# Kernel tuning notes

Hardware: AMD Instinct MI355X
Metric: run time of the kernel (lower is better)

## Reference

```python
import jax, jax.numpy as jnp
import numpy as np

TAU = 1.0  # temperaturesa
GRID = 5   # torch.chunk(..., 5) along H and W


def _cam(X, gamma, tau):
    # Channel attention: energy = Xf Xf^T over spatial dim, with max-subtraction/negation trick.
    B, C, H, W = X.shape
    Xf = X.reshape(B, C, H * W)
    energy = jnp.einsum('bcn,bdn->bcd', Xf, Xf)                      # [B,C,C]
    energy_new = jnp.max(energy, axis=-1, keepdims=True) - energy
    attn = jax.nn.softmax(energy_new / tau, axis=-1)
    out = jnp.einsum('bcd,bdn->bcn', attn, Xf).reshape(B, C, H, W)
    return gamma * out + X


def _pam(X, Wq, bq, Wk, bk, Wv, bv, gamma, tau):
    # Position attention with 1x1-conv q/k/v (1x1 conv == channel matmul).
    B, C, H, W = X.shape
    N = H * W
    Xf = X.reshape(B, C, N)
    q = jnp.einsum('kc,bcn->bnk', Wq, Xf) + bq                        # [B,N,C//8]
    k = jnp.einsum('kc,bcn->bkn', Wk, Xf) + bk[None, :, None]         # [B,C//8,N]
    v = jnp.einsum('dc,bcn->bdn', Wv, Xf) + bv[None, :, None]         # [B,C,N]
    energy = jnp.einsum('bnk,bkm->bnm', q, k)                         # [B,N,N]
    attn = jax.nn.softmax(energy / tau, axis=-1)
    # torch: bmm(value, attention.permute(0,2,1)) -> out[b,d,m] = sum_n v[b,d,n]*attn[b,m,n]
    out = jnp.einsum('bdn,bmn->bdm', v, attn).reshape(B, C, H, W)
    return gamma * out + X


def _cka_loss(X, Y):
    # linear_CKA_loss: HKH centering done as K - rowmean - colmean + totalmean.
    def cgram(Z):
        K = Z @ Z.T                                                   # [B,B]
        rm = jnp.mean(K, axis=1, keepdims=True)
        cm = jnp.mean(K, axis=0, keepdims=True)
        return K - rm - cm + jnp.mean(K)
    cX, cY = cgram(X), cgram(Y)
    hsic = jnp.sum(cX * cY)
    v1 = jnp.sqrt(jnp.sum(cX * cX))
    v2 = jnp.sqrt(jnp.sum(cY * cY))
    return -jnp.log(jnp.abs(hsic / (v1 * v2)) + 1e-8)


def _grid_chunks(X, g=GRID):
    # 5x5 spatial tiling -> [g*g, B, C, H/g, W/g]
    B, C, H, W = X.shape
    h, w = H // g, W // g
    return X.reshape(B, C, g, h, g, w).transpose(2, 4, 0, 1, 3, 5).reshape(g * g, B, C, h, w)


def setup_inputs() -> dict:
    key = jax.random.key(0)
    ks = jax.random.split(key, 10)
    B, C, H, W = 16, 256, 80, 80
    Ck = C // 8
    return {
        'feat_S': jax.random.normal(ks[0], (B, C, H, W), jnp.float32),
        'feat_T': jax.random.normal(ks[1], (B, C, H, W), jnp.float32),
        'Wq': jax.random.normal(ks[2], (Ck, C), jnp.float32),
        'bq': jax.random.normal(ks[3], (Ck,), jnp.float32),
        'Wk': jax.random.normal(ks[4], (Ck, C), jnp.float32),
        'bk': jax.random.normal(ks[5], (Ck,), jnp.float32),
        'Wv': jax.random.normal(ks[6], (C, C), jnp.float32),
        'bv': jax.random.normal(ks[7], (C,), jnp.float32),
        'gammacam': jax.random.normal(ks[8], (1,), jnp.float32),
        'gammapam': jax.random.normal(ks[9], (1,), jnp.float32),
    }


def reference(feat_S, feat_T, Wq, bq, Wk, bk, Wv, bv, gammacam, gammapam):
    # feature_transform == 'separately_CAMgridPAM_CKA'
    tau = TAU
    pam = lambda X: _pam(X, Wq, bq, Wk, bk, Wv, bv, gammapam, tau)
    chunks_S = _grid_chunks(feat_S)                                   # [25,B,C,16,16]
    chunks_T = _grid_chunks(feat_T)
    pam_S = jax.vmap(pam)(chunks_S)
    pam_T = jax.vmap(pam)(chunks_T)
    nchunk, B = pam_S.shape[0], pam_S.shape[1]
    flat_S = pam_S.reshape(nchunk, B, -1)
    flat_T = pam_T.reshape(nchunk, B, -1)
    loss_PAM = jnp.mean(jax.vmap(_cka_loss)(flat_S, flat_T))          # sum/n == mean
    CAM_S = _cam(feat_S, gammacam, tau)
    CAM_T = _cam(feat_T, gammacam, tau)
    loss_CAM = _cka_loss(CAM_S.reshape(B, -1), CAM_T.reshape(B, -1))
    return (loss_CAM, loss_PAM)
```

## Files before the change

### kernel.cpp

```cpp
#include <hip/hip_runtime.h>


typedef short bf16x8 __attribute__((ext_vector_type(8)));
typedef float f32x4 __attribute__((ext_vector_type(4)));

constexpr int BB = 16;
constexpr int CH = 256;
constexpr int HW = 6400;
constexpr int IMW = 80;

__device__ __forceinline__ int lds_off(int row, int half, int k2) {
  return row * 128 + ((((half << 6)) | k2) ^ ((row & 7) << 4));
}

__device__ __forceinline__ bf16x8 frag_ld(const char* base, int row, int half, int lane) {
  int off = row * 128 + ((((half << 6)) | ((lane >> 4) << 4)) ^ ((lane & 7) << 4));
  return *(const bf16x8*)(base + off);
}

__device__ __forceinline__ void cvt2(float x, unsigned short& h, unsigned short& l) {
  unsigned u = __float_as_uint(x);
  h = (unsigned short)(u >> 16);
  float r = x - __uint_as_float(u & 0xffff0000u);
  l = (unsigned short)(__float_as_uint(r) >> 16);
}

__device__ __forceinline__ void cvt4(float4 v, ushort4& h, ushort4& l) {
  cvt2(v.x, h.x, l.x); cvt2(v.y, h.y, l.y);
  cvt2(v.z, h.z, l.z); cvt2(v.w, h.w, l.w);
}

__device__ __forceinline__ void cvt8(float4 v0, float4 v1, bf16x8& hi, bf16x8& lo) {
  unsigned short h, l;
  cvt2(v0.x, h, l); hi[0] = (short)h; lo[0] = (short)l;
  cvt2(v0.y, h, l); hi[1] = (short)h; lo[1] = (short)l;
  cvt2(v0.z, h, l); hi[2] = (short)h; lo[2] = (short)l;
  cvt2(v0.w, h, l); hi[3] = (short)h; lo[3] = (short)l;
  cvt2(v1.x, h, l); hi[4] = (short)h; lo[4] = (short)l;
  cvt2(v1.y, h, l); hi[5] = (short)h; lo[5] = (short)l;
  cvt2(v1.z, h, l); hi[6] = (short)h; lo[6] = (short)l;
  cvt2(v1.w, h, l); hi[7] = (short)h; lo[7] = (short)l;
}

__device__ __forceinline__ unsigned short bf_rnd(float x) {
  unsigned u = __float_as_uint(x);
  return (unsigned short)((u + 0x8000u) >> 16);
}

__global__ __launch_bounds__(1024) void cam_energy_k(const float* __restrict__ fS,
                                                     const float* __restrict__ fT,
                                                     float* __restrict__ part) {
  const int kc = blockIdx.x, b = blockIdx.y, t = blockIdx.z;
  const float* X = (t ? fT : fS) + (size_t)b * CH * HW;
  __shared__ unsigned short lds[2 * 256 * 64];
  const int tid = threadIdx.x, lane = tid & 63, w = tid >> 6;
  const int wr = w >> 2, wc = w & 3;
  const int r0 = tid >> 2, kq = tid & 3;
  const int half = kq >> 1, k2b = (kq & 1) * 32;
  const float* Xr = X + (size_t)r0 * HW + kc * 800 + kq * 16;
  f32x4 acc[4][4] = {};
  float4 v[4];
#pragma unroll
  for (int q = 0; q < 4; ++q) v[q] = *(const float4*)(Xr + q * 4);
  for (int it = 0; it < 13; ++it) {
    char* pb = (char*)lds + (it & 1) * 32768;
#pragma unroll
    for (int q = 0; q < 4; ++q) {
      ushort4 u;
      u.x = bf_rnd(v[q].x); u.y = bf_rnd(v[q].y);
      u.z = bf_rnd(v[q].z); u.w = bf_rnd(v[q].w);
      *(ushort4*)(pb + lds_off(r0, half, k2b + q * 8)) = u;
    }
    __syncthreads();
    float4 nv[4];
    if (it < 12) {
      const int nk = (it + 1) * 64;
      if (nk + kq * 16 < 800) {
        const float* Xn = Xr + nk;
#pragma unroll
        for (int q = 0; q < 4; ++q) nv[q] = *(const float4*)(Xn + q * 4);
      } else {
#pragma unroll
        for (int q = 0; q < 4; ++q) nv[q] = make_float4(0.f, 0.f, 0.f, 0.f);
      }
    }
#pragma unroll
    for (int h = 0; h < 2; ++h) {
      bf16x8 bh[4];
#pragma unroll
      for (int n = 0; n < 4; ++n)
        bh[n] = frag_ld(pb, wc * 64 + n * 16 + (lane & 15), h, lane);
#pragma unroll
      for (int m = 0; m < 4; ++m) {
        bf16x8 a = frag_ld(pb, wr * 64 + m * 16 + (lane & 15), h, lane);
#pragma unroll
        for (int n = 0; n < 4; ++n)
          acc[m][n] = __builtin_amdgcn_mfma_f32_16x16x32_bf16(a, bh[n], acc[m][n], 0, 0, 0);
      }
    }
#pragma unroll
    for (int q = 0; q < 4; ++q) v[q] = nv[q];
  }
  float* Eb = part + (((size_t)kc * 2 + t) * BB + b) * 65536;
#pragma unroll
  for (int m = 0; m < 4; ++m)
#pragma unroll
    for (int n = 0; n < 4; ++n) {
      int row = wr * 64 + m * 16 + ((lane >> 4) << 2);
      int col = wc * 64 + n * 16 + (lane & 15);
#pragma unroll
      for (int r2 = 0; r2 < 4; ++r2)
        Eb[(size_t)(row + r2) * 256 + col] = acc[m][n][r2];
    }
}

__global__ __launch_bounds__(64) void cam_softmax_k(float* __restrict__ part) {
  const int c = blockIdx.x, b = blockIdx.y, t = blockIdx.z;
  const size_t base = (((size_t)t * BB + b) * CH + c) * CH;
  const int lane = threadIdx.x;
  float4 x = make_float4(0.f, 0.f, 0.f, 0.f);
#pragma unroll
  for (int p = 0; p < 8; ++p) {
    float4 y = ((const float4*)(part + (size_t)p * 2097152 + base))[lane];
    x.x += y.x; x.y += y.y; x.z += y.z; x.w += y.w;
  }
  float mn = fminf(fminf(x.x, x.y), fminf(x.z, x.w));
  for (int o = 32; o; o >>= 1) mn = fminf(mn, __shfl_xor(mn, o));
  float4 p4;
  p4.x = __expf(mn - x.x); p4.y = __expf(mn - x.y);
  p4.z = __expf(mn - x.z); p4.w = __expf(mn - x.w);
  float s = (p4.x + p4.y) + (p4.z + p4.w);
  for (int o = 32; o; o >>= 1) s += __shfl_xor(s, o);
  const float inv = 1.0f / s;
  p4.x *= inv; p4.y *= inv; p4.z *= inv; p4.w *= inv;
  ((float4*)(part + base))[lane] = p4;
}

template <int MODE>
__global__ __launch_bounds__(1024) void ax_k(const float* __restrict__ Abase, int Astride,
                                             const float* __restrict__ X,
                                             float* __restrict__ OUT,
                                             const float* __restrict__ bvec,
                                             const float* __restrict__ gsc) {
  const int nt = blockIdx.x;
  const int b = blockIdx.y;
  const float* A = Abase + (size_t)b * Astride;
  const float* Xb = X + (size_t)b * CH * HW;
  float* OUTb = OUT + (size_t)b * CH * HW;
  const int nbase = nt * 128;
  __shared__ unsigned short lds[2 * (256 + 128) * 64];
  const int tid = threadIdx.x, lane = tid & 63, w = tid >> 6;
  const int wr = w >> 2, wc = w & 3;
  const int r0 = tid >> 2, kq = tid & 3;
  const int n_r = tid & 127, kg = tid >> 7;
  const float* Xcol = Xb + nbase + n_r;
  f32x4 acc[4][2] = {};
  float4 ra[2];
  float vb4[4];
#pragma unroll
  for (int q = 0; q < 2; ++q)
    ra[q] = *(const float4*)(A + (size_t)r0 * 256 + kq * 8 + q * 4);
#pragma unroll
  for (int e = 0; e < 4; ++e)
    vb4[e] = Xcol[(size_t)(kg * 4 + e) * HW];
  for (int s = 0; s < 8; ++s) {
    char* Ab = (char*)lds + (s & 1) * 49152;
    char* Bb = Ab + 32768;
#pragma unroll
    for (int q = 0; q < 2; ++q) {
      ushort4 h4, l4;
      cvt4(ra[q], h4, l4);
      *(ushort4*)(Ab + lds_off(r0, 0, kq * 16 + q * 8)) = h4;
      *(ushort4*)(Ab + lds_off(r0, 1, kq * 16 + q * 8)) = l4;
    }
    {
      unsigned short bh[4], bl[4];
#pragma unroll
      for (int e = 0; e < 4; ++e) cvt2(vb4[e], bh[e], bl[e]);
      *(ushort4*)(Bb + lds_off(n_r, 0, kg * 8)) = make_ushort4(bh[0], bh[1], bh[2], bh[3]);
      *(ushort4*)(Bb + lds_off(n_r, 1, kg * 8)) = make_ushort4(bl[0], bl[1], bl[2], bl[3]);
    }
    __syncthreads();
    if (s < 7) {
      int k0 = (s + 1) * 32;
#pragma unroll
      for (int q = 0; q < 2; ++q)
        ra[q] = *(const float4*)(A + (size_t)r0 * 256 + k0 + kq * 8 + q * 4);
#pragma unroll
      for (int e = 0; e < 4; ++e)
        vb4[e] = Xcol[(size_t)(k0 + kg * 4 + e) * HW];
    }
    bf16x8 bfr[2][2];
#pragma unroll
    for (int h = 0; h < 2; ++h)
#pragma unroll
      for (int n = 0; n < 2; ++n)
        bfr[h][n] = frag_ld(Bb, wc * 32 + n * 16 + (lane & 15), h, lane);
#pragma unroll
    for (int m = 0; m < 4; ++m) {
      int arow = wr * 64 + m * 16 + (lane & 15);
      bf16x8 a0 = frag_ld(Ab, arow, 0, lane);
      bf16x8 a1 = frag_ld(Ab, arow, 1, lane);
#pragma unroll
      for (int n = 0; n < 2; ++n)
        acc[m][n] = __builtin_amdgcn_mfma_f32_16x16x32_bf16(a0, bfr[0][n], acc[m][n], 0, 0, 0);
#pragma unroll
      for (int n = 0; n < 2; ++n)
        acc[m][n] = __builtin_amdgcn_mfma_f32_16x16x32_bf16(a0, bfr[1][n], acc[m][n], 0, 0, 0);
#pragma unroll
      for (int n = 0; n < 2; ++n)
        acc[m][n] = __builtin_amdgcn_mfma_f32_16x16x32_bf16(a1, bfr[0][n], acc[m][n], 0, 0, 0);
    }
  }
  float g = 0.f;
  if (MODE == 0) g = gsc[0];
#pragma unroll
  for (int m = 0; m < 4; ++m)
#pragma unroll
    for (int n = 0; n < 2; ++n) {
      int row = wr * 64 + m * 16 + ((lane >> 4) << 2);
      int col = nbase + wc * 32 + n * 16 + (lane & 15);
#pragma unroll
      for (int r2 = 0; r2 < 4; ++r2) {
        size_t o = (size_t)(row + r2) * HW + col;
        float v = acc[m][n][r2];
        if (MODE == 0) OUTb[o] = g * v + Xb[o];
        else           OUTb[o] = v + bvec[row + r2];
      }
    }
}

__global__ __launch_bounds__(256) void qk_k(const float* __restrict__ X,
                                            const float* __restrict__ Wq,
                                            const float* __restrict__ bq,
                                            const float* __restrict__ Wk,
                                            const float* __restrict__ bk,
                                            float* __restrict__ qt,
                                            float* __restrict__ kf) {
  const int nbase = blockIdx.x * 256;
  const int b = blockIdx.y;
  const float* Xb = X + (size_t)b * CH * HW;
  __shared__ unsigned short lds[(64 + 256) * 64];
  char* Ab = (char*)lds;
  char* Bb = (char*)lds + 8192;
  const int tid = threadIdx.x, lane = tid & 63, w = tid >> 6;
  const int ar = tid >> 2, akq = tid & 3;
  const int n4 = (tid & 63) * 4, c0l = tid >> 6;
  const float* Arow = (ar < 32) ? (Wq + (size_t)ar * CH) : (Wk + (size_t)(ar - 32) * CH);
  f32x4 acc[4][4] = {};
  float4 va[2], vb[8];
#pragma unroll
  for (int q = 0; q < 2; ++q)
    va[q] = *(const float4*)(Arow + akq * 8 + q * 4);
#pragma unroll
  for (int q = 0; q < 8; ++q)
    vb[q] = *(const float4*)(Xb + (size_t)(c0l + 4 * q) * HW + nbase + n4);
  for (int s = 0; s < 8; ++s) {
    __syncthreads();
#pragma unroll
    for (int q = 0; q < 2; ++q) {
      ushort4 h4, l4;
      cvt4(va[q], h4, l4);
      *(ushort4*)(Ab + lds_off(ar, 0, akq * 16 + q * 8)) = h4;
      *(ushort4*)(Ab + lds_off(ar, 1, akq * 16 + q * 8)) = l4;
    }
#pragma unroll
    for (int q = 0; q < 8; ++q) {
      int cc = c0l + 4 * q;
      float4 v = vb[q];
#pragma unroll
      for (int jj = 0; jj < 4; ++jj) {
        int j = (jj + tid) & 3;
        float e = (j == 0) ? v.x : (j == 1) ? v.y : (j == 2) ? v.z : v.w;
        unsigned short h, l;
        cvt2(e, h, l);
        int row = n4 + j;
        *(unsigned short*)(Bb + lds_off(row, 0, cc * 2)) = h;
        *(unsigned short*)(Bb + lds_off(row, 1, cc * 2)) = l;
      }
    }
    __syncthreads();
    float4 na[2], nb[8];
    if (s < 7) {
      const int k0 = (s + 1) * 32;
#pragma unroll
      for (int q = 0; q < 2; ++q)
        na[q] = *(const float4*)(Arow + k0 + akq * 8 + q * 4);
#pragma unroll
      for (int q = 0; q < 8; ++q)
        nb[q] = *(const float4*)(Xb + (size_t)(k0 + c0l + 4 * q) * HW + nbase + n4);
    }
    bf16x8 bfr[2][4];
#pragma unroll
    for (int h = 0; h < 2; ++h)
#pragma unroll
      for (int n = 0; n < 4; ++n)
        bfr[h][n] = frag_ld(Bb, w * 64 + n * 16 + (lane & 15), h, lane);
#pragma unroll
    for (int m = 0; m < 4; ++m) {
      int arow2 = m * 16 + (lane & 15);
      bf16x8 a0 = frag_ld(Ab, arow2, 0, lane);
      bf16x8 a1 = frag_ld(Ab, arow2, 1, lane);
#pragma unroll
      for (int n = 0; n < 4; ++n)
        acc[m][n] = __builtin_amdgcn_mfma_f32_16x16x32_bf16(a0, bfr[0][n], acc[m][n], 0, 0, 0);
#pragma unroll
      for (int n = 0; n < 4; ++n)
        acc[m][n] = __builtin_amdgcn_mfma_f32_16x16x32_bf16(a0, bfr[1][n], acc[m][n], 0, 0, 0);
#pragma unroll
      for (int n = 0; n < 4; ++n)
        acc[m][n] = __builtin_amdgcn_mfma_f32_16x16x32_bf16(a1, bfr[0][n], acc[m][n], 0, 0, 0);
    }
#pragma unroll
    for (int q = 0; q < 2; ++q) va[q] = na[q];
#pragma unroll
    for (int q = 0; q < 8; ++q) vb[q] = nb[q];
  }
#pragma unroll
  for (int m = 0; m < 4; ++m)
#pragma unroll
    for (int n = 0; n < 4; ++n) {
      int row = m * 16 + ((lane >> 4) << 2);
      int col = nbase + w * 64 + n * 16 + (lane & 15);
#pragma unroll
      for (int r2 = 0; r2 < 4; ++r2) {
        int rr = row + r2;
        float v = acc[m][n][r2];
        if (rr < 32) qt[((size_t)b * HW + col) * 32 + rr] = v + bq[rr];
        else         kf[((size_t)b * 32 + (rr - 32)) * HW + col] = v + bk[rr - 32];
      }
    }
}

__global__ __launch_bounds__(256) void pam_es_k(const float* __restrict__ qt,
                                                const float* __restrict__ kf,
                                                float* __restrict__ Pbuf) {
  const int ccb = blockIdx.x;
  const int ck = ccb >> 4, b = ccb & 15;
  const int gi = ck / 5, gj = ck % 5;
  const int pbase = gi * 16 * IMW + gj * 16;
  float* Pc = Pbuf + (size_t)ccb * 65536;
  __shared__ float qs[256][32];
  __shared__ float S[32][256];
  const int tid = threadIdx.x;
  const float* qb = qt + (size_t)b * HW * 32;
#pragma unroll
  for (int qq = 0; qq < 8; ++qq) {
    int j = (tid >> 3) + 32 * qq;
    int nj = pbase + (j >> 4) * IMW + (j & 15);
    float4 v = *(const float4*)(qb + (size_t)nj * 32 + (tid & 7) * 4);
    *(float4*)&qs[j][(tid & 7) * 4] = v;
  }
  const int nt = pbase + (tid >> 4) * IMW + (tid & 15);
  const float* kb = kf + (size_t)b * 32 * HW;
  float kc[32];
#pragma unroll
  for (int kk = 0; kk < 32; ++kk) kc[kk] = kb[(size_t)kk * HW + nt];
  __syncthreads();
  const int w = tid >> 6, lane = tid & 63;
  for (int p = 0; p < 8; ++p) {
#pragma unroll 4
    for (int j2 = 0; j2 < 32; ++j2) {
      int row = p * 32 + j2;
      float s = 0.f;
#pragma unroll
      for (int k8 = 0; k8 < 8; ++k8) {
        float4 qv = *(const float4*)&qs[row][k8 * 4];
        s = fmaf(qv.x, kc[k8 * 4 + 0], s);
        s = fmaf(qv.y, kc[k8 * 4 + 1], s);
        s = fmaf(qv.z, kc[k8 * 4 + 2], s);
        s = fmaf(qv.w, kc[k8 * 4 + 3], s);
      }
      S[j2][tid] = s;
    }
    __syncthreads();
#pragma unroll
    for (int rr = 0; rr < 8; ++rr) {
      int jj = w * 8 + rr;
      float4 v = *(const float4*)&S[jj][lane << 2];
      float m = fmaxf(fmaxf(v.x, v.y), fmaxf(v.z, v.w));
      for (int o = 32; o; o >>= 1) m = fmaxf(m, __shfl_xor(m, o));
      float4 pv;
      pv.x = __expf(v.x - m); pv.y = __expf(v.y - m);
      pv.z = __expf(v.z - m); pv.w = __expf(v.w - m);
      float s = (pv.x + pv.y) + (pv.z + pv.w);
      for (int o = 32; o; o >>= 1) s += __shfl_xor(s, o);
      const float inv = 1.f / s;
      pv.x *= inv; pv.y *= inv; pv.z *= inv; pv.w *= inv;
      *(float4*)&Pc[(size_t)(p * 32 + jj) * 256 + (lane << 2)] = pv;
    }
    __syncthreads();
  }
}

__global__ __launch_bounds__(512) void pam_pv_k(float* __restrict__ P,
                                                const float* __restrict__ V,
                                                const float* __restrict__ fS,
                                                const float* __restrict__ fT,
                                                const float* __restrict__ gsc, int t) {
  const int ccb = blockIdx.x;
  const int ck = ccb >> 4, b = ccb & 15;
  const int gi = ck / 5, gj = ck % 5;
  const float* Xb = (t ? fT : fS) + (size_t)b * CH * HW;
  const float* Vb = V + (size_t)b * CH * HW;
  float* Pc = P + (size_t)ccb * 65536;
  __shared__ unsigned short lds[2 * 256 * 64];
  char* Ab = (char*)lds;
  char* Bb = (char*)lds + 32768;
  const int tid = threadIdx.x, lane = tid & 63, w = tid >> 6;
  const int wr = w >> 2, wc = w & 3;
  const int r0 = tid >> 3, kq = tid & 7;
  const int pbase = gi * 16 * IMW + gj * 16;
  f32x4 acc[8][4] = {};
  float4 va[4], vb[4];
  {
    int jj = kq * 4;
    int ngl = pbase + (jj >> 4) * IMW + (jj & 15);
#pragma unroll
    for (int q = 0; q < 4; ++q) {
      int rr = r0 + 64 * q;
      va[q] = *(const float4*)(Vb + (size_t)rr * HW + ngl);
      vb[q] = *(const float4*)(Pc + (size_t)rr * 256 + kq * 4);
    }
  }
  for (int s = 0; s < 8; ++s) {
    __syncthreads();
#pragma unroll
    for (int q = 0; q < 4; ++q) {
      int rr = r0 + 64 * q;
      ushort4 h4, l4;
      cvt4(va[q], h4, l4);
      *(ushort4*)(Ab + lds_off(rr, 0, kq * 8)) = h4;
      *(ushort4*)(Ab + lds_off(rr, 1, kq * 8)) = l4;
      cvt4(vb[q], h4, l4);
      *(ushort4*)(Bb + lds_off(rr, 0, kq * 8)) = h4;
      *(ushort4*)(Bb + lds_off(rr, 1, kq * 8)) = l4;
    }
    __syncthreads();
    float4 na[4], nb[4];
    if (s < 7) {
      int k0 = (s + 1) * 32;
      int jj = k0 + kq * 4;
      int ngl = pbase + (jj >> 4) * IMW + (jj & 15);
#pragma unroll
      for (int q = 0; q < 4; ++q) {
        int rr = r0 + 64 * q;
        na[q] = *(const float4*)(Vb + (size_t)rr * HW + ngl);
        nb[q] = *(const float4*)(Pc + (size_t)rr * 256 + k0 + kq * 4);
      }
    }
    bf16x8 bfr[2][4];
#pragma unroll
    for (int h = 0; h < 2; ++h)
#pragma unroll
      for (int n = 0; n < 4; ++n)
        bfr[h][n] = frag_ld(Bb, wc * 64 + n * 16 + (lane & 15), h, lane);
#pragma unroll
    for (int m = 0; m < 8; ++m) {
      int arow = wr * 128 + m * 16 + (lane & 15);
      bf16x8 a0 = frag_ld(Ab, arow, 0, lane);
      bf16x8 a1 = frag_ld(Ab, arow, 1, lane);
#pragma unroll
      for (int n = 0; n < 4; ++n)
        acc[m][n] = __builtin_amdgcn_mfma_f32_16x16x32_bf16(a0, bfr[0][n], acc[m][n], 0, 0, 0);
#pragma unroll
      for (int n = 0; n < 4; ++n)
        acc[m][n] = __builtin_amdgcn_mfma_f32_16x16x32_bf16(a0, bfr[1][n], acc[m][n], 0, 0, 0);
#pragma unroll
      for (int n = 0; n < 4; ++n)
        acc[m][n] = __builtin_amdgcn_mfma_f32_16x16x32_bf16(a1, bfr[0][n], acc[m][n], 0, 0, 0);
    }
#pragma unroll
    for (int q = 0; q < 4; ++q) { va[q] = na[q]; vb[q] = nb[q]; }
  }
  const float g = gsc[0];
#pragma unroll
  for (int m = 0; m < 8; ++m)
#pragma unroll
    for (int n = 0; n < 4; ++n) {
      int row = wr * 128 + m * 16 + ((lane >> 4) << 2);
      int col = wc * 64 + n * 16 + (lane & 15);
      int ngl = pbase + (col >> 4) * IMW + (col & 15);
#pragma unroll
      for (int r2 = 0; r2 < 4; ++r2) {
        float v = g * acc[m][n][r2] + Xb[(size_t)(row + r2) * HW + ngl];
        Pc[(size_t)(row + r2) * 256 + col] = v;
      }
    }
}

__global__ __launch_bounds__(256) void gram_mfma_k(const float* __restrict__ Z,
                                                   size_t gStride, size_t bStride,
                                                   double* __restrict__ G) {
  const int tid = threadIdx.x, lane = tid & 63, w = tid >> 6;
  const float* Zg = Z + (size_t)blockIdx.y * gStride;
  const float* p = Zg + (size_t)(lane & 15) * bStride +
                   (size_t)blockIdx.x * 4096 + w * 1024 + ((lane >> 4) << 3);
  f32x4 acc = {};
#pragma unroll 4
  for (int s = 0; s < 32; ++s) {
    float4 v0 = *(const float4*)(p + s * 32);
    float4 v1 = *(const float4*)(p + s * 32 + 4);
    bf16x8 hi, lo;
    cvt8(v0, v1, hi, lo);
    acc = __builtin_amdgcn_mfma_f32_16x16x32_bf16(hi, hi, acc, 0, 0, 0);
    acc = __builtin_amdgcn_mfma_f32_16x16x32_bf16(hi, lo, acc, 0, 0, 0);
    acc = __builtin_amdgcn_mfma_f32_16x16x32_bf16(lo, hi, acc, 0, 0, 0);
  }
  double* Gt = G + (size_t)blockIdx.y * 256;
  const int col = lane & 15, row0 = (lane >> 4) << 2;
#pragma unroll
  for (int i = 0; i < 4; ++i)
    atomicAdd(&Gt[(size_t)(row0 + i) * 16 + col], (double)acc[i]);
}

__global__ __launch_bounds__(256) void cka_pair_k(const double* __restrict__ G,
                                                  double* __restrict__ losses) {
  const int q = blockIdx.x;
  const double* KX = (q == 0) ? G : G + 512 + (size_t)(q - 1) * 256;
  const double* KY = (q == 0) ? G + 256 : G + 512 + 6400 + (size_t)(q - 1) * 256;
  __shared__ double red[256];
  __shared__ double srm[16], scm[16];
  __shared__ double stm;
  const int tid = threadIdx.x;
  const int r = tid >> 4, c = tid & 15;

  auto center = [&](double k) -> double {
    red[tid] = k;
    __syncthreads();
    for (int off = 8; off; off >>= 1) {
      if (c < off) red[tid] += red[tid + off];
      __syncthreads();
    }
    if (c == 0) srm[r] = red[tid] * (1.0 / 16.0);
    __syncthreads();
    red[c * 16 + r] = k;
    __syncthreads();
    for (int off = 8; off; off >>= 1) {
      if (r < off) red[c * 16 + r] += red[c * 16 + r + off];
      __syncthreads();
    }
    if (r == 0) scm[c] = red[c * 16] * (1.0 / 16.0);
    __syncthreads();
    if (tid == 0) {
      double s = 0.0;
      for (int i = 0; i < 16; ++i) s += srm[i];
      stm = s * (1.0 / 16.0);
    }
    __syncthreads();
    double v = k - srm[r] - scm[c] + stm;
    __syncthreads();
    return v;
  };
  auto reduce_sum = [&](double v) -> double {
    red[tid] = v;
    __syncthreads();
    for (int off = 128; off; off >>= 1) {
      if (tid < off) red[tid] += red[tid + off];
      __syncthreads();
    }
    double s = red[0];
    __syncthreads();
    return s;
  };
  double cx = center(KX[tid]);
  double cy = center(KY[tid]);
  double h = reduce_sum(cx * cy);
  double v1 = reduce_sum(cx * cx);
  double v2 = reduce_sum(cy * cy);
  if (tid == 0) losses[q] = -log(fabs(h / (sqrt(v1) * sqrt(v2))) + 1e-8);
}

__global__ void cka_combine_k(const double* __restrict__ losses,
                              float* __restrict__ out) {
  if (threadIdx.x == 0) {
    out[0] = (float)losses[0];
    double s = 0.0;
    for (int q = 1; q <= 25; ++q) s += losses[q];
    out[1] = (float)(s * (1.0 / 25.0));
  }
}

extern "C" void kernel_launch(void* const* d_in, const int* in_sizes, int n_in,
                              void* d_out, int out_size, void* d_ws, size_t ws_size,
                              hipStream_t stream) {
  (void)in_sizes; (void)n_in; (void)out_size; (void)ws_size;
  const float* fS = (const float*)d_in[0];
  const float* fT = (const float*)d_in[1];
  const float* Wq = (const float*)d_in[2];
  const float* bq = (const float*)d_in[3];
  const float* Wk = (const float*)d_in[4];
  const float* bk = (const float*)d_in[5];
  const float* Wv = (const float*)d_in[6];
  const float* bv = (const float*)d_in[7];
  const float* gcam = (const float*)d_in[8];
  const float* gpam = (const float*)d_in[9];
  float* out = (float*)d_out;

  float* buf0 = (float*)d_ws;
  float* buf1 = buf0 + 26214400;
  double* G = (double*)(buf1 + 26214400);
  float* Pbuf = buf1;
  float* qt = buf0;
  float* kf = buf0 + 3276800;
  double* losses = (double*)buf0;

  hipMemsetAsync(G, 0, 13312 * sizeof(double), stream);

  cam_energy_k<<<dim3(8, 16, 2), 1024, 0, stream>>>(fS, fT, buf1);
  cam_softmax_k<<<dim3(256, 16, 2), 64, 0, stream>>>(buf1);
  for (int t = 0; t < 2; ++t) {
    ax_k<0><<<dim3(50, 16), 1024, 0, stream>>>(buf1 + (size_t)t * BB * 65536, 65536,
                                               t ? fT : fS, buf0, nullptr, gcam);
    gram_mfma_k<<<dim3(400, 1), 256, 0, stream>>>(buf0, (size_t)0, (size_t)1638400,
                                                  G + t * 256);
  }
  for (int t = 0; t < 2; ++t) {
    const float* X = t ? fT : fS;
    qk_k<<<dim3(25, 16), 256, 0, stream>>>(X, Wq, bq, Wk, bk, qt, kf);
    pam_es_k<<<dim3(400), 256, 0, stream>>>(qt, kf, Pbuf);
    ax_k<1><<<dim3(50, 16), 1024, 0, stream>>>(Wv, 0, X, buf0, bv, nullptr);
    pam_pv_k<<<dim3(400), 512, 0, stream>>>(Pbuf, buf0, fS, fT, gpam, t);
    gram_mfma_k<<<dim3(16, 25), 256, 0, stream>>>(Pbuf, (size_t)1048576, (size_t)65536,
                                                  G + 512 + t * 6400);
  }
  cka_pair_k<<<dim3(26), 256, 0, stream>>>(G, losses);
  cka_combine_k<<<dim3(1), 64, 0, stream>>>(losses, out);
}
```

Baseline: 1.001 ms.

## Double-buffer LDS in PAM PV kernel and widen block to 1024 threads

The PAM value-times-attention kernel now runs 16 waves per block instead of 8, halving per-wave accumulator tiles (4x4 instead of 8x4) and loading 8 floats per thread per row. LDS is double-buffered by step parity, which drops one __syncthreads per k-step. The MFMA loop is reordered so that each B half-fragment is loaded once per pass. The aim is more latency hiding, lower register pressure and fewer barriers, at the cost of twice the shared memory per block (128KB), which may limit blocks per CU.

```diff
diff --git a/kernel.cpp b/kernel.cpp
--- a/kernel.cpp
+++ b/kernel.cpp
@@ -393,92 +393,88 @@
   }
 }
 
-__global__ __launch_bounds__(512) void pam_pv_k(float* __restrict__ P,
-                                                const float* __restrict__ V,
-                                                const float* __restrict__ fS,
-                                                const float* __restrict__ fT,
-                                                const float* __restrict__ gsc, int t) {
+__global__ __launch_bounds__(1024) void pam_pv_k(float* __restrict__ P,
+                                                 const float* __restrict__ V,
+                                                 const float* __restrict__ fS,
+                                                 const float* __restrict__ fT,
+                                                 const float* __restrict__ gsc, int t) {
   const int ccb = blockIdx.x;
   const int ck = ccb >> 4, b = ccb & 15;
   const int gi = ck / 5, gj = ck % 5;
   const float* Xb = (t ? fT : fS) + (size_t)b * CH * HW;
   const float* Vb = V + (size_t)b * CH * HW;
   float* Pc = P + (size_t)ccb * 65536;
-  __shared__ unsigned short lds[2 * 256 * 64];
-  char* Ab = (char*)lds;
-  char* Bb = (char*)lds + 32768;
+  __shared__ unsigned short lds[2 * 2 * 256 * 64];
   const int tid = threadIdx.x, lane = tid & 63, w = tid >> 6;
   const int wr = w >> 2, wc = w & 3;
-  const int r0 = tid >> 3, kq = tid & 7;
+  const int r0 = tid >> 2, kq = tid & 3;
   const int pbase = gi * 16 * IMW + gj * 16;
-  f32x4 acc[8][4] = {};
-  float4 va[4], vb[4];
+  f32x4 acc[4][4] = {};
+  float4 va[2], vb[2];
   {
-    int jj = kq * 4;
+    int jj = kq * 8;
     int ngl = pbase + (jj >> 4) * IMW + (jj & 15);
-#pragma unroll
-    for (int q = 0; q < 4; ++q) {
-      int rr = r0 + 64 * q;
-      va[q] = *(const float4*)(Vb + (size_t)rr * HW + ngl);
-      vb[q] = *(const float4*)(Pc + (size_t)rr * 256 + kq * 4);
-    }
+    va[0] = *(const float4*)(Vb + (size_t)r0 * HW + ngl);
+    va[1] = *(const float4*)(Vb + (size_t)r0 * HW + ngl + 4);
+    vb[0] = *(const float4*)(Pc + (size_t)r0 * 256 + jj);
+    vb[1] = *(const float4*)(Pc + (size_t)r0 * 256 + jj + 4);
   }
   for (int s = 0; s < 8; ++s) {
-    __syncthreads();
-#pragma unroll
-    for (int q = 0; q < 4; ++q) {
-      int rr = r0 + 64 * q;
+    char* Ab = (char*)lds + (s & 1) * 65536;
+    char* Bb = Ab + 32768;
+    {
       ushort4 h4, l4;
-      cvt4(va[q], h4, l4);
-      *(ushort4*)(Ab + lds_off(rr, 0, kq * 8)) = h4;
-      *(ushort4*)(Ab + lds_off(rr, 1, kq * 8)) = l4;
-      cvt4(vb[q], h4, l4);
-      *(ushort4*)(Bb + lds_off(rr, 0, kq * 8)) = h4;
-      *(ushort4*)(Bb + lds_off(rr, 1, kq * 8)) = l4;
-    }
-    __syncthreads();
-    float4 na[4], nb[4];
+      cvt4(va[0], h4, l4);
+      *(ushort4*)(Ab + lds_off(r0, 0, kq * 16)) = h4;
+      *(ushort4*)(Ab + lds_off(r0, 1, kq * 16)) = l4;
+      cvt4(va[1], h4, l4);
+      *(ushort4*)(Ab + lds_off(r0, 0, kq * 16 + 8)) = h4;
+      *(ushort4*)(Ab + lds_off(r0, 1, kq * 16 + 8)) = l4;
+      cvt4(vb[0], h4, l4);
+      *(ushort4*)(Bb + lds_off(r0, 0, kq * 16)) = h4;
+      *(ushort4*)(Bb + lds_off(r0, 1, kq * 16)) = l4;
+      cvt4(vb[1], h4, l4);
+      *(ushort4*)(Bb + lds_off(r0, 0, kq * 16 + 8)) = h4;
+      *(ushort4*)(Bb + lds_off(r0, 1, kq * 16 + 8)) = l4;
+    }
+    __syncthreads();
     if (s < 7) {
       int k0 = (s + 1) * 32;
-      int jj = k0 + kq * 4;
+      int jj = k0 + kq * 8;
       int ngl = pbase + (jj >> 4) * IMW + (jj & 15);
-#pragma unroll
-      for (int q = 0; q < 4; ++q) {
-        int rr = r0 + 64 * q;
-        na[q] = *(const float4*)(Vb + (size_t)rr * HW + ngl);
-        nb[q] = *(const float4*)(Pc + (size_t)rr * 256 + k0 + kq * 4);
-      }
-    }
-    bf16x8 bfr[2][4];
-#pragma unroll
-    for (int h = 0; h < 2; ++h)
+      va[0] = *(const float4*)(Vb + (size_t)r0 * HW + ngl);
+      va[1] = *(const float4*)(Vb + (size_t)r0 * HW + ngl + 4);
+      vb[0] = *(const float4*)(Pc + (size_t)r0 * 256 + k0 + kq * 8);
+      vb[1] = *(const float4*)(Pc + (size_t)r0 * 256 + k0 + kq * 8 + 4);
+    }
+#pragma unroll
+    for (int hb = 0; hb < 2; ++hb) {
+      bf16x8 bh[4];
 #pragma unroll
       for (int n = 0; n < 4; ++n)
-        bfr[h][n] = frag_ld(Bb, wc * 64 + n * 16 + (lane & 15), h, lane);
-#pragma unroll
-    for (int m = 0; m < 8; ++m) {
-      int arow = wr * 128 + m * 16 + (lane & 15);
-      bf16x8 a0 = frag_ld(Ab, arow, 0, lane);
-      bf16x8 a1 = frag_ld(Ab, arow, 1, lane);
-#pragma unroll
-      for (int n = 0; n < 4; ++n)
-        acc[m][n] = __builtin_amdgcn_mfma_f32_16x16x32_bf16(a0, bfr[0][n], acc[m][n], 0, 0, 0);
-#pragma unroll
-      for (int n = 0; n < 4; ++n)
-        acc[m][n] = __builtin_amdgcn_mfma_f32_16x16x32_bf16(a0, bfr[1][n], acc[m][n], 0, 0, 0);
-#pragma unroll
-      for (int n = 0; n < 4; ++n)
-        acc[m][n] = __builtin_amdgcn_mfma_f32_16x16x32_bf16(a1, bfr[0][n], acc[m][n], 0, 0, 0);
-    }
-#pragma unroll
-    for (int q = 0; q < 4; ++q) { va[q] = na[q]; vb[q] = nb[q]; }
+        bh[n] = frag_ld(Bb, wc * 64 + n * 16 + (lane & 15), hb, lane);
+#pragma unroll
+      for (int m = 0; m < 4; ++m) {
+        int arow = wr * 64 + m * 16 + (lane & 15);
+        bf16x8 a0 = frag_ld(Ab, arow, 0, lane);
+#pragma unroll
+        for (int n = 0; n < 4; ++n)
+          acc[m][n] = __builtin_amdgcn_mfma_f32_16x16x32_bf16(a0, bh[n], acc[m][n], 0, 0, 0);
+        if (hb == 0) {
+          bf16x8 a1 = frag_ld(Ab, arow, 1, lane);
+#pragma unroll
+          for (int n = 0; n < 4; ++n)
+            acc[m][n] = __builtin_amdgcn_mfma_f32_16x16x32_bf16(a1, bh[n], acc[m][n], 0, 0, 0);
+        }
+      }
+    }
   }
   const float g = gsc[0];
 #pragma unroll
-  for (int m = 0; m < 8; ++m)
+  for (int m = 0; m < 4; ++m)
 #pragma unroll
     for (int n = 0; n < 4; ++n) {
-      int row = wr * 128 + m * 16 + ((lane >> 4) << 2);
+      int row = wr * 64 + m * 16 + ((lane >> 4) << 2);
       int col = wc * 64 + n * 16 + (lane & 15);
       int ngl = pbase + (col >> 4) * IMW + (col & 15);
 #pragma unroll
@@ -620,7 +616,7 @@
     qk_k<<<dim3(25, 16), 256, 0, stream>>>(X, Wq, bq, Wk, bk, qt, kf);
     pam_es_k<<<dim3(400), 256, 0, stream>>>(qt, kf, Pbuf);
     ax_k<1><<<dim3(50, 16), 1024, 0, stream>>>(Wv, 0, X, buf0, bv, nullptr);
-    pam_pv_k<<<dim3(400), 512, 0, stream>>>(Pbuf, buf0, fS, fT, gpam, t);
+    pam_pv_k<<<dim3(400), 1024, 0, stream>>>(Pbuf, buf0, fS, fT, gpam, t);
     gram_mfma_k<<<dim3(16, 25), 256, 0, stream>>>(Pbuf, (size_t)1048576, (size_t)65536,
                                                   G + 512 + t * 6400);
   }
```

Result: no change. 993.5 us (median of 4 runs) (-0.7%).
